# Kernel optimization log

Hardware: AMD Instinct MI355X
Metric: run time of the kernel (lower is better)

## Reference

```python
import jax, jax.numpy as jnp
import numpy as np

EMBED = 192
D_INNER = 2 * EMBED          # expand=2
D_STATE = 4                  # low_rank
D_CONV = 4
DT_RANK = (EMBED + 15) // 16 # ceil(192/16) = 12
N_MIX = 2
RANK = 4                     # LowRankProjection rank
B_, H_, W_ = 8, 64, 64


def setup_inputs() -> dict:
    key = jax.random.key(0)
    ks = jax.random.split(key, 16)
    s = lambda *sh: 1.0 / np.sqrt(sh[-1])
    inp = {
        "x": jax.random.normal(ks[0], (B_, EMBED, H_, W_), jnp.float32),
        # stacked per-mixer Mamba params (leading dim N_MIX)
        "in_proj_w": jax.random.normal(ks[1], (N_MIX, 2 * D_INNER, EMBED), jnp.float32) * s(EMBED),
        "conv_w": jax.random.normal(ks[2], (N_MIX, D_INNER, D_CONV), jnp.float32) * s(D_CONV),
        "conv_b": jnp.zeros((N_MIX, D_INNER), jnp.float32),
        "x_proj_w": jax.random.normal(ks[3], (N_MIX, DT_RANK + 2 * D_STATE, D_INNER), jnp.float32) * s(D_INNER),
        "dt_proj_w": jax.random.normal(ks[4], (N_MIX, D_INNER, DT_RANK), jnp.float32) * s(DT_RANK),
        "dt_proj_b": jax.random.uniform(ks[5], (N_MIX, D_INNER), jnp.float32, -4.0, -2.0),
        "A_log": jnp.tile(jnp.log(jnp.arange(1, D_STATE + 1, dtype=jnp.float32))[None, None, :], (N_MIX, D_INNER, 1)),
        "D": jnp.ones((N_MIX, D_INNER), jnp.float32),
        "out_proj_w": jax.random.normal(ks[6], (N_MIX, EMBED, D_INNER), jnp.float32) * s(D_INNER),
        # LowRankProjection
        "U_w": jax.random.normal(ks[7], (RANK, EMBED), jnp.float32) * s(EMBED),
        "V_w": jax.random.normal(ks[8], (EMBED, RANK), jnp.float32) * s(RANK),
        # LayerNorm
        "ln_g": jnp.ones((EMBED,), jnp.float32),
        "ln_b": jnp.zeros((EMBED,), jnp.float32),
    }
    return inp


def _silu(x):
    return x * jax.nn.sigmoid(x)


def _mamba(x, in_proj_w, conv_w, conv_b, x_proj_w, dt_proj_w, dt_proj_b, A_log, D, out_proj_w):
    # x: (B, L, d_model)
    B, L, _ = x.shape
    xz = jnp.einsum("bld,ed->ble", x, in_proj_w)          # (B, L, 2*d_inner)
    xin, z = jnp.split(xz, 2, axis=-1)
    # causal depthwise conv over L
    xt = jnp.transpose(xin, (0, 2, 1))                      # (B, d_inner, L)
    xc = jax.lax.conv_general_dilated(
        xt, conv_w[:, None, :], window_strides=(1,), padding=[(D_CONV - 1, 0)],
        feature_group_count=D_INNER, dimension_numbers=("NCH", "OIH", "NCH"))
    xa = _silu(jnp.transpose(xc + conv_b[None, :, None], (0, 2, 1)))  # (B, L, d_inner)
    x_dbl = jnp.einsum("bld,ed->ble", xa, x_proj_w)         # (B, L, dt_rank+2*d_state)
    dt_lr = x_dbl[..., :DT_RANK]
    Bm = x_dbl[..., DT_RANK:DT_RANK + D_STATE]              # (B, L, d_state)
    Cm = x_dbl[..., DT_RANK + D_STATE:]                     # (B, L, d_state)
    dt = jax.nn.softplus(jnp.einsum("blr,dr->bld", dt_lr, dt_proj_w) + dt_proj_b)  # (B, L, d_inner)
    A = -jnp.exp(A_log)                                     # (d_inner, d_state)
    dA = jnp.exp(dt[..., None] * A)                         # (B, L, d_inner, d_state)
    dBu = dt[..., None] * Bm[:, :, None, :] * xa[..., None]  # (B, L, d_inner, d_state)

    def step(h, inputs):
        dA_i, dBu_i, C_i = inputs                           # (B,d_inner,d_state),(B,d_inner,d_state),(B,d_state)
        h = dA_i * h + dBu_i
        y = jnp.einsum("bds,bs->bd", h, C_i)
        return h, y

    h0 = jnp.zeros((B, D_INNER, D_STATE), x.dtype)
    _, ys = jax.lax.scan(step, h0, (jnp.moveaxis(dA, 1, 0), jnp.moveaxis(dBu, 1, 0), jnp.moveaxis(Cm, 1, 0)))
    y = jnp.moveaxis(ys, 0, 1) + xa * D                     # (B, L, d_inner)
    y = y * _silu(z)
    return jnp.einsum("ble,de->bld", y, out_proj_w)         # (B, L, d_model)


def reference(x, in_proj_w, conv_w, conv_b, x_proj_w, dt_proj_w, dt_proj_b,
              A_log, D, out_proj_w, U_w, V_w, ln_g, ln_b):
    residual = x
    B, C, H, W = x.shape
    h = jnp.transpose(x, (0, 2, 3, 1)).reshape(B, H * W, C)
    for i in range(N_MIX):
        h = _mamba(h, in_proj_w[i], conv_w[i], conv_b[i], x_proj_w[i], dt_proj_w[i],
                   dt_proj_b[i], A_log[i], D[i], out_proj_w[i])
    # low-rank projection
    h = jnp.einsum("blr,dr->bld", jnp.einsum("blc,rc->blr", h, U_w), V_w)
    h = jnp.transpose(h.reshape(B, H, W, C), (0, 3, 1, 2)) + residual
    # LayerNorm over channels
    hc = jnp.transpose(h, (0, 2, 3, 1))
    mu = hc.mean(-1, keepdims=True)
    var = ((hc - mu) ** 2).mean(-1, keepdims=True)
    hc = (hc - mu) * jax.lax.rsqrt(var + 1e-5) * ln_g + ln_b
    return jnp.transpose(hc, (0, 3, 1, 2))
```

## Files before the change

### kernel.cpp

```cpp
#include <hip/hip_runtime.h>
#include <hip/hip_bf16.h>
#include <cstdint>

#define EMBED   192
#define DINNER  384
#define DSTATE  4
#define DCONV   4
#define DTRANK  12
#define NMIX    2
#define RANK    4
#define BB      8
#define LL      4096
#define NBL     (BB*LL)
#define NCHUNK  128
#define CLEN    32

typedef __attribute__((ext_vector_type(8))) short short8;
typedef __attribute__((ext_vector_type(4))) float float4v;

static __device__ __forceinline__ ushort f2b(float f) {
    __hip_bfloat16 h = __float2bfloat16(f);
    return *(ushort*)&h;
}
static __device__ __forceinline__ float b2f(ushort u) {
    __hip_bfloat16 h;
    *(ushort*)&h = u;
    return __bfloat162float(h);
}
static __device__ __forceinline__ float bs2f(short s) {
    ushort u = (ushort)s;
    return b2f(u);
}

__global__ __launch_bounds__(256) void k_cast(const float* __restrict__ src,
                                              ushort* __restrict__ dst, int n) {
    int i = blockIdx.x * 256 + threadIdx.x;
    if (i < n) dst[i] = f2b(src[i]);
}

__global__ __launch_bounds__(256) void k_pad_xpw(const float* __restrict__ src,
                                                 ushort* __restrict__ dst) {
    int i = blockIdx.x * 256 + threadIdx.x;
    if (i >= NMIX * 32 * 384) return;
    int mix = i / (32 * 384);
    int rem = i % (32 * 384);
    int e = rem / 384, k = rem % 384;
    dst[i] = (e < 20) ? f2b(src[(size_t)mix * 20 * 384 + e * 384 + k]) : (ushort)0;
}

__global__ __launch_bounds__(256) void k_pad_dtw(const float* __restrict__ src,
                                                 ushort* __restrict__ dst) {
    int i = blockIdx.x * 256 + threadIdx.x;
    if (i >= NMIX * 384 * 32) return;
    int mix = i / (384 * 32);
    int rem = i % (384 * 32);
    int n = rem / 32, r = rem % 32;
    dst[i] = (r < DTRANK) ? f2b(src[(size_t)mix * 384 * DTRANK + n * DTRANK + r]) : (ushort)0;
}

__global__ __launch_bounds__(256) void k_prep_cwt(const float* __restrict__ src,
                                                  float* __restrict__ dst) {
    int i = blockIdx.x * 256 + threadIdx.x;
    if (i >= NMIX * DCONV * DINNER) return;
    int mix = i / (DCONV * DINNER);
    int rem = i % (DCONV * DINNER);
    int k = rem / DINNER, d = rem % DINNER;
    dst[i] = src[(size_t)mix * DINNER * DCONV + d * DCONV + k];
}

__global__ __launch_bounds__(256) void k_transpose(const float* __restrict__ x,
                                                   ushort* __restrict__ h0b) {
    __shared__ float tile[32][33];
    int b  = blockIdx.z;
    int c0 = blockIdx.y * 32;
    int l0 = blockIdx.x * 32;
    int tx = threadIdx.x;
    int ty = threadIdx.y;
    #pragma unroll
    for (int i = 0; i < 4; i++) {
        int c = c0 + ty + i * 8;
        tile[ty + i * 8][tx] = x[((size_t)b * EMBED + c) * LL + l0 + tx];
    }
    __syncthreads();
    #pragma unroll
    for (int i = 0; i < 4; i++) {
        int l = l0 + ty + i * 8;
        h0b[((size_t)b * LL + l) * EMBED + c0 + tx] = f2b(tile[tx][ty + i * 8]);
    }
}

template<int TN, int WRN>
__global__ __launch_bounds__(256) void k_gemm_bf16(const ushort* __restrict__ A, int lda,
                                                   const ushort* __restrict__ Bw, int ldb,
                                                   float* __restrict__ C, int ldc,
                                                   ushort* __restrict__ Cb, int ldcb,
                                                   int K) {
    constexpr int WRM = 4 / WRN;
    constexpr int WM  = 128 / WRM;
    constexpr int MT  = WM / 16;
    __shared__ ushort As[128][40];
    __shared__ ushort Bs[TN][40];
    int tid  = threadIdx.x;
    int lane = tid & 63;
    int wave = tid >> 6;
    int wmo = (wave / WRN) * WM;
    int wno = (wave % WRN) * 64;
    int m0 = blockIdx.y * 128;
    int n0 = blockIdx.x * TN;

    float4v acc[MT][4];
    #pragma unroll
    for (int i = 0; i < MT; i++)
        #pragma unroll
        for (int j = 0; j < 4; j++)
            acc[i][j] = (float4v){0.f, 0.f, 0.f, 0.f};

    for (int k0 = 0; k0 < K; k0 += 32) {
        #pragma unroll
        for (int i = 0; i < 2; i++) {
            int idx = tid + i * 256;
            int r = idx >> 2, sg = idx & 3;
            *(short8*)&As[r][sg * 8] =
                *(const short8*)(A + (size_t)(m0 + r) * lda + k0 + sg * 8);
        }
        #pragma unroll
        for (int i = 0; i < TN / 64; i++) {
            int idx = tid + i * 256;
            int r = idx >> 2, sg = idx & 3;
            *(short8*)&Bs[r][sg * 8] =
                *(const short8*)(Bw + (size_t)(n0 + r) * ldb + k0 + sg * 8);
        }
        __syncthreads();
        short8 av[MT], bv[4];
        #pragma unroll
        for (int i = 0; i < MT; i++)
            av[i] = *(const short8*)&As[wmo + i * 16 + (lane & 15)][(lane >> 4) * 8];
        #pragma unroll
        for (int j = 0; j < 4; j++)
            bv[j] = *(const short8*)&Bs[wno + j * 16 + (lane & 15)][(lane >> 4) * 8];
        #pragma unroll
        for (int i = 0; i < MT; i++)
            #pragma unroll
            for (int j = 0; j < 4; j++)
                acc[i][j] = __builtin_amdgcn_mfma_f32_16x16x32_bf16(
                    av[i], bv[j], acc[i][j], 0, 0, 0);
        __syncthreads();
    }

    #pragma unroll
    for (int i = 0; i < MT; i++) {
        int rbase = m0 + wmo + i * 16 + (lane >> 4) * 4;
        #pragma unroll
        for (int j = 0; j < 4; j++) {
            int col = n0 + wno + j * 16 + (lane & 15);
            #pragma unroll
            for (int r = 0; r < 4; r++) {
                float v = acc[i][j][r];
                if (C)  C[(size_t)(rbase + r) * ldc + col] = v;
                if (Cb) Cb[(size_t)(rbase + r) * ldcb + col] = f2b(v);
            }
        }
    }
}

__global__ __launch_bounds__(256) void k_conv_silu(const ushort* __restrict__ xz,
                                                   const float* __restrict__ cwt,
                                                   const float* __restrict__ cb,
                                                   ushort* __restrict__ xa) {
    int t   = blockIdx.x * 256 + threadIdx.x;
    int g   = t % 48;
    int blc = t / 48;
    int d0  = g * 8;
    int lc  = blc % (LL / 8);
    int b   = blc / (LL / 8);
    int l0  = lc * 8;

    float wk[4][8], bias[8];
    #pragma unroll
    for (int k = 0; k < 4; k++) {
        float4v wa = *(const float4v*)(cwt + k * DINNER + d0);
        float4v wb = *(const float4v*)(cwt + k * DINNER + d0 + 4);
        #pragma unroll
        for (int j = 0; j < 4; j++) { wk[k][j] = wa[j]; wk[k][j + 4] = wb[j]; }
    }
    {
        float4v ba = *(const float4v*)(cb + d0);
        float4v bb = *(const float4v*)(cb + d0 + 4);
        #pragma unroll
        for (int j = 0; j < 4; j++) { bias[j] = ba[j]; bias[j + 4] = bb[j]; }
    }

    float r0[8] = {}, r1[8] = {}, r2[8] = {};
    const ushort* px = xz + ((size_t)(b * LL + l0)) * 768 + d0;
    if (l0 > 0) {
        short8 v;
        v = *(const short8*)(px - 3 * 768);
        #pragma unroll
        for (int j = 0; j < 8; j++) r0[j] = bs2f(v[j]);
        v = *(const short8*)(px - 2 * 768);
        #pragma unroll
        for (int j = 0; j < 8; j++) r1[j] = bs2f(v[j]);
        v = *(const short8*)(px - 1 * 768);
        #pragma unroll
        for (int j = 0; j < 8; j++) r2[j] = bs2f(v[j]);
    }
    ushort* po = xa + ((size_t)(b * LL + l0)) * DINNER + d0;
    #pragma unroll
    for (int i = 0; i < 8; i++) {
        short8 v = *(const short8*)(px + (size_t)i * 768);
        float cur[8];
        #pragma unroll
        for (int j = 0; j < 8; j++) cur[j] = bs2f(v[j]);
        short8 ov;
        #pragma unroll
        for (int j = 0; j < 8; j++) {
            float a = bias[j] + wk[0][j] * r0[j] + wk[1][j] * r1[j]
                    + wk[2][j] * r2[j] + wk[3][j] * cur[j];
            float sv = a / (1.f + __expf(-a));
            ov[j] = (short)f2b(sv);
        }
        *(short8*)(po + (size_t)i * DINNER) = ov;
        #pragma unroll
        for (int j = 0; j < 8; j++) { r0[j] = r1[j]; r1[j] = r2[j]; r2[j] = cur[j]; }
    }
}

__global__ __launch_bounds__(256) void k_xproj_mfma(const ushort* __restrict__ xa,
                                                    const ushort* __restrict__ xpwb,
                                                    float* __restrict__ xdb32,
                                                    ushort* __restrict__ xdb16) {
    __shared__ ushort As[128][40];
    __shared__ ushort Bs[32][40];
    int tid  = threadIdx.x;
    int lane = tid & 63;
    int wave = tid >> 6;
    int m0 = blockIdx.x * 128;
    float4v acc[2][2];
    #pragma unroll
    for (int i = 0; i < 2; i++)
        #pragma unroll
        for (int j = 0; j < 2; j++)
            acc[i][j] = (float4v){0.f, 0.f, 0.f, 0.f};
    for (int k0 = 0; k0 < 384; k0 += 32) {
        #pragma unroll
        for (int i = 0; i < 2; i++) {
            int idx = tid + i * 256;
            int r = idx >> 2, sg = idx & 3;
            *(short8*)&As[r][sg * 8] =
                *(const short8*)(xa + (size_t)(m0 + r) * 384 + k0 + sg * 8);
        }
        if (tid < 128) {
            int r = tid >> 2, sg = tid & 3;
            *(short8*)&Bs[r][sg * 8] =
                *(const short8*)(xpwb + (size_t)r * 384 + k0 + sg * 8);
        }
        __syncthreads();
        short8 av[2], bv[2];
        #pragma unroll
        for (int i = 0; i < 2; i++)
            av[i] = *(const short8*)&As[wave * 32 + i * 16 + (lane & 15)][(lane >> 4) * 8];
        #pragma unroll
        for (int j = 0; j < 2; j++)
            bv[j] = *(const short8*)&Bs[j * 16 + (lane & 15)][(lane >> 4) * 8];
        #pragma unroll
        for (int i = 0; i < 2; i++)
            #pragma unroll
            for (int j = 0; j < 2; j++)
                acc[i][j] = __builtin_amdgcn_mfma_f32_16x16x32_bf16(
                    av[i], bv[j], acc[i][j], 0, 0, 0);
        __syncthreads();
    }
    #pragma unroll
    for (int i = 0; i < 2; i++) {
        int rbase = m0 + wave * 32 + i * 16 + (lane >> 4) * 4;
        #pragma unroll
        for (int j = 0; j < 2; j++) {
            int col = j * 16 + (lane & 15);
            #pragma unroll
            for (int r = 0; r < 4; r++) {
                float v = acc[i][j][r];
                xdb32[(size_t)(rbase + r) * 32 + col] = v;
                xdb16[(size_t)(rbase + r) * 32 + col] = f2b(v);
            }
        }
    }
}

__global__ __launch_bounds__(256) void k_dtgemm(const ushort* __restrict__ xdb16,
                                                const ushort* __restrict__ dtwpad,
                                                const float* __restrict__ dtb,
                                                ushort* __restrict__ dtv) {
    int lane = threadIdx.x & 63;
    int wave = threadIdx.x >> 6;
    int m0 = blockIdx.x * 64 + wave * 16;
    int ak = (lane >> 4) * 8;
    short8 av = *(const short8*)(xdb16 + (size_t)(m0 + (lane & 15)) * 32 + ak);
    int rbase = m0 + (lane >> 4) * 4;
    #pragma unroll
    for (int j = 0; j < 24; j++) {
        int col = j * 16 + (lane & 15);
        short8 bv = *(const short8*)(dtwpad + (size_t)col * 32 + ak);
        float4v acc = (float4v){0.f, 0.f, 0.f, 0.f};
        acc = __builtin_amdgcn_mfma_f32_16x16x32_bf16(av, bv, acc, 0, 0, 0);
        float bias = dtb[col];
        #pragma unroll
        for (int r = 0; r < 4; r++) {
            float s = acc[r] + bias;
            float sp = fmaxf(s, 0.f) + __logf(1.f + __expf(-fabsf(s)));
            dtv[(size_t)(rbase + r) * DINNER + col] = f2b(sp);
        }
    }
}

__global__ __launch_bounds__(384) void k_scan_local(const ushort* __restrict__ xa,
                                                    const float* __restrict__ xdb32,
                                                    const ushort* __restrict__ dtvb,
                                                    const float* __restrict__ A_log,
                                                    float* __restrict__ carryT,
                                                    float* __restrict__ carryH) {
    int d     = threadIdx.x;
    int chunk = blockIdx.x;
    int b     = blockIdx.y;
    __shared__ float rows[CLEN * 32];
    size_t rbase = ((size_t)b * LL + (size_t)chunk * CLEN) * 32;
    for (int i = d; i < CLEN * 32; i += 384) rows[i] = xdb32[rbase + i];
    float As[DSTATE];
    #pragma unroll
    for (int s = 0; s < DSTATE; s++) As[s] = -__expf(A_log[d * DSTATE + s]);
    __syncthreads();
    float h[DSTATE] = {0.f, 0.f, 0.f, 0.f};
    float T = 0.f;
    size_t mbase = (size_t)b * LL + (size_t)chunk * CLEN;
    for (int l = 0; l < CLEN; l++) {
        size_t m = mbase + l;
        float dtvv = b2f(dtvb[m * DINNER + d]);
        float xav  = b2f(xa[m * DINNER + d]);
        float du   = dtvv * xav;
        T += dtvv;
        const float* row = &rows[l * 32];
        #pragma unroll
        for (int s = 0; s < DSTATE; s++) {
            float da = __expf(dtvv * As[s]);
            h[s] = da * h[s] + du * row[DTRANK + s];
        }
    }
    size_t cb = ((size_t)chunk * BB + b);
    carryT[cb * 384 + d] = T;
    float4v hv = {h[0], h[1], h[2], h[3]};
    *(float4v*)(carryH + cb * 1536 + d * 4) = hv;
}

__global__ __launch_bounds__(256) void k_scan_combine(const float* __restrict__ carryT,
                                                      const float* __restrict__ carryH,
                                                      const float* __restrict__ A_log,
                                                      float* __restrict__ carryI) {
    int c   = blockIdx.x * 256 + threadIdx.x;
    int b   = c / 1536;
    int rem = c - b * 1536;
    int d   = rem >> 2;
    float As = -__expf(A_log[rem]);
    float hrun = 0.f;
    for (int k = 0; k < NCHUNK; k++) {
        size_t o = (size_t)k * BB + b;
        float T  = carryT[o * 384 + d];
        float Hk = carryH[o * 1536 + rem];
        carryI[o * 1536 + rem] = hrun;
        hrun = __expf(As * T) * hrun + Hk;
    }
}

__global__ __launch_bounds__(384) void k_scan_final(const ushort* __restrict__ xa,
                                                    const ushort* __restrict__ xz,
                                                    const float* __restrict__ xdb32,
                                                    const ushort* __restrict__ dtvb,
                                                    const float* __restrict__ A_log,
                                                    const float* __restrict__ Dp,
                                                    const float* __restrict__ carryI,
                                                    ushort* __restrict__ y) {
    int d     = threadIdx.x;
    int chunk = blockIdx.x;
    int b     = blockIdx.y;
    __shared__ float rows[CLEN * 32];
    size_t rbase = ((size_t)b * LL + (size_t)chunk * CLEN) * 32;
    for (int i = d; i < CLEN * 32; i += 384) rows[i] = xdb32[rbase + i];
    float As[DSTATE];
    #pragma unroll
    for (int s = 0; s < DSTATE; s++) As[s] = -__expf(A_log[d * DSTATE + s]);
    float Dd = Dp[d];
    float4v hv = *(const float4v*)(carryI + ((size_t)chunk * BB + b) * 1536 + d * 4);
    float h[DSTATE];
    #pragma unroll
    for (int s = 0; s < DSTATE; s++) h[s] = hv[s];
    __syncthreads();
    size_t mbase = (size_t)b * LL + (size_t)chunk * CLEN;
    for (int l = 0; l < CLEN; l++) {
        size_t m = mbase + l;
        float dtvv = b2f(dtvb[m * DINNER + d]);
        float xav  = b2f(xa[m * DINNER + d]);
        float du   = dtvv * xav;
        const float* row = &rows[l * 32];
        float yv = 0.f;
        #pragma unroll
        for (int s = 0; s < DSTATE; s++) {
            float da = __expf(dtvv * As[s]);
            h[s] = da * h[s] + du * row[DTRANK + s];
            yv  += h[s] * row[DTRANK + DSTATE + s];
        }
        yv += xav * Dd;
        float zv = b2f(xz[m * 768 + DINNER + d]);
        yv *= zv / (1.f + __expf(-zv));
        y[m * DINNER + d] = f2b(yv);
    }
}

__global__ __launch_bounds__(256) void k_tail(const ushort* __restrict__ h1b,
                                              const float* __restrict__ x,
                                              const float* __restrict__ U,
                                              const float* __restrict__ V,
                                              const float* __restrict__ g,
                                              const float* __restrict__ be,
                                              float* __restrict__ out) {
    __shared__ float tile[EMBED * 65];
    int tid  = threadIdx.x;
    int lane = tid & 63;
    int wave = tid >> 6;
    int b  = blockIdx.y;
    int l0 = blockIdx.x * 64;
    for (int i = tid; i < EMBED * 64; i += 256) {
        int c = i >> 6, l = i & 63;
        tile[c * 65 + l] = x[((size_t)(b * EMBED + c)) * LL + l0 + l];
    }
    __syncthreads();
    for (int t = 0; t < 16; t++) {
        int lloc = wave * 16 + t;
        size_t m = (size_t)b * LL + l0 + lloc;
        float hv[3];
        #pragma unroll
        for (int i = 0; i < 3; i++) hv[i] = b2f(h1b[m * EMBED + lane + 64 * i]);
        float r[RANK];
        #pragma unroll
        for (int j = 0; j < RANK; j++) {
            float p = 0.f;
            #pragma unroll
            for (int i = 0; i < 3; i++) p += hv[i] * U[j * EMBED + lane + 64 * i];
            #pragma unroll
            for (int off = 1; off < 64; off <<= 1) p += __shfl_xor(p, off);
            r[j] = p;
        }
        float u[3], s1 = 0.f, s2 = 0.f;
        #pragma unroll
        for (int i = 0; i < 3; i++) {
            int c = lane + 64 * i;
            float v = r[0] * V[c * 4 + 0] + r[1] * V[c * 4 + 1]
                    + r[2] * V[c * 4 + 2] + r[3] * V[c * 4 + 3];
            u[i] = v + tile[c * 65 + lloc];
            s1 += u[i];
            s2 += u[i] * u[i];
        }
        #pragma unroll
        for (int off = 1; off < 64; off <<= 1) {
            s1 += __shfl_xor(s1, off);
            s2 += __shfl_xor(s2, off);
        }
        float mean = s1 * (1.f / EMBED);
        float var  = s2 * (1.f / EMBED) - mean * mean;
        float inv  = rsqrtf(var + 1e-5f);
        #pragma unroll
        for (int i = 0; i < 3; i++) {
            int c = lane + 64 * i;
            tile[c * 65 + lloc] = (u[i] - mean) * inv * g[c] + be[c];
        }
    }
    __syncthreads();
    for (int i = tid; i < EMBED * 64; i += 256) {
        int c = i >> 6, l = i & 63;
        out[((size_t)(b * EMBED + c)) * LL + l0 + l] = tile[c * 65 + l];
    }
}

extern "C" void kernel_launch(void* const* d_in, const int* in_sizes, int n_in,
                              void* d_out, int out_size, void* d_ws, size_t ws_size,
                              hipStream_t stream) {
    const float* x          = (const float*)d_in[0];
    const float* in_proj_w  = (const float*)d_in[1];
    const float* conv_w     = (const float*)d_in[2];
    const float* conv_b     = (const float*)d_in[3];
    const float* x_proj_w   = (const float*)d_in[4];
    const float* dt_proj_w  = (const float*)d_in[5];
    const float* dt_proj_b  = (const float*)d_in[6];
    const float* A_log      = (const float*)d_in[7];
    const float* Dp         = (const float*)d_in[8];
    const float* out_proj_w = (const float*)d_in[9];
    const float* U_w        = (const float*)d_in[10];
    const float* V_w        = (const float*)d_in[11];
    const float* ln_g       = (const float*)d_in[12];
    const float* ln_b       = (const float*)d_in[13];
    float* out = (float*)d_out;

    float* ws    = (float*)d_ws;
    float* xdb32 = ws;
    float* carryT = xdb32 + (size_t)NBL * 32;
    float* carryH = carryT + (size_t)NCHUNK * BB * DINNER;
    float* carryI = carryH + (size_t)NCHUNK * BB * DINNER * DSTATE;
    ushort* dtv    = (ushort*)(carryI + (size_t)NCHUNK * BB * DINNER * DSTATE);
    ushort* xz16   = dtv    + (size_t)NBL * DINNER;
    ushort* xa16   = xz16   + (size_t)NBL * 768;
    ushort* yb     = xa16   + (size_t)NBL * DINNER;
    ushort* h0b    = yb     + (size_t)NBL * DINNER;
    ushort* h1b    = h0b    + (size_t)NBL * EMBED;
    ushort* wi     = h1b    + (size_t)NBL * EMBED;
    ushort* wo     = wi     + (size_t)NMIX * 768 * EMBED;
    ushort* xpwb   = wo     + (size_t)NMIX * EMBED * DINNER;
    ushort* dtwpad = xpwb   + (size_t)NMIX * 32 * 384;
    float*  cwt    = (float*)(dtwpad + (size_t)NMIX * 384 * 32);

    const int n_wi = NMIX * 768 * EMBED;
    const int n_wo = NMIX * EMBED * DINNER;
    k_cast<<<(n_wi + 255) / 256, 256, 0, stream>>>(in_proj_w, wi, n_wi);
    k_cast<<<(n_wo + 255) / 256, 256, 0, stream>>>(out_proj_w, wo, n_wo);
    k_pad_xpw<<<(NMIX * 32 * 384 + 255) / 256, 256, 0, stream>>>(x_proj_w, xpwb);
    k_pad_dtw<<<(NMIX * 384 * 32 + 255) / 256, 256, 0, stream>>>(dt_proj_w, dtwpad);
    k_prep_cwt<<<(NMIX * DCONV * DINNER + 255) / 256, 256, 0, stream>>>(conv_w, cwt);

    k_transpose<<<dim3(LL / 32, EMBED / 32, BB), dim3(32, 8), 0, stream>>>(x, h0b);

    const ushort* hinb = h0b;
    for (int mix = 0; mix < NMIX; mix++) {
        const float* Alg = A_log + (size_t)mix * DINNER * DSTATE;

        k_gemm_bf16<128, 2><<<dim3(768 / 128, NBL / 128), 256, 0, stream>>>(
            hinb, EMBED, wi + (size_t)mix * 768 * EMBED, EMBED,
            (float*)nullptr, 0, xz16, 768, EMBED);
        k_conv_silu<<<(NBL / 8 * 48) / 256, 256, 0, stream>>>(
            xz16, cwt + (size_t)mix * DCONV * DINNER, conv_b + mix * DINNER, xa16);
        ushort* xdb16 = yb;
        k_xproj_mfma<<<NBL / 128, 256, 0, stream>>>(
            xa16, xpwb + (size_t)mix * 32 * 384, xdb32, xdb16);
        k_dtgemm<<<NBL / 64, 256, 0, stream>>>(
            xdb16, dtwpad + (size_t)mix * 384 * 32, dt_proj_b + mix * DINNER, dtv);
        k_scan_local<<<dim3(NCHUNK, BB), 384, 0, stream>>>(
            xa16, xdb32, dtv, Alg, carryT, carryH);
        k_scan_combine<<<(BB * DINNER * DSTATE) / 256, 256, 0, stream>>>(
            carryT, carryH, Alg, carryI);
        k_scan_final<<<dim3(NCHUNK, BB), 384, 0, stream>>>(
            xa16, xz16, xdb32, dtv, Alg, Dp + mix * DINNER, carryI, yb);
        k_gemm_bf16<64, 1><<<dim3(EMBED / 64, NBL / 128), 256, 0, stream>>>(
            yb, DINNER, wo + (size_t)mix * EMBED * DINNER, DINNER,
            (float*)nullptr, 0, h1b, EMBED, DINNER);
        hinb = h1b;
    }

    k_tail<<<dim3(LL / 64, BB), 256, 0, stream>>>(h1b, x, U_w, V_w, ln_g, ln_b, out);
}
```

Baseline: 428.7 us.

## Fuse weight prep kernels, fuse x_proj with dt_proj, read residual from bf16 copy

Merges the five weight cast and pad kernels into one launch. Fuses the x_proj GEMM with the dt_proj GEMM and softplus by staging the bf16 x_proj output in shared memory, so the intermediate no longer goes through global memory and one launch per mixer is removed. The tail kernel now reads the residual from the already-transposed bf16 copy h0b instead of re-transposing the fp32 input through shared memory. The residual therefore carries bf16 rounding, which lowers output accuracy.

```diff
diff --git a/kernel.cpp b/kernel.cpp
--- a/kernel.cpp
+++ b/kernel.cpp
@@ -32,40 +32,55 @@
     return b2f(u);
 }
 
-__global__ __launch_bounds__(256) void k_cast(const float* __restrict__ src,
-                                              ushort* __restrict__ dst, int n) {
+#define PREP_N0 294912
+#define PREP_N1 147456
+#define PREP_N2 24576
+#define PREP_N3 24576
+#define PREP_N4 3072
+__global__ __launch_bounds__(256) void k_prep(const float* __restrict__ in_proj_w,
+                                              const float* __restrict__ out_proj_w,
+                                              const float* __restrict__ x_proj_w,
+                                              const float* __restrict__ dt_proj_w,
+                                              const float* __restrict__ conv_w,
+                                              ushort* __restrict__ wi,
+                                              ushort* __restrict__ wo,
+                                              ushort* __restrict__ xpwb,
+                                              ushort* __restrict__ dtwpad,
+                                              float* __restrict__ cwt) {
     int i = blockIdx.x * 256 + threadIdx.x;
-    if (i < n) dst[i] = f2b(src[i]);
-}
-
-__global__ __launch_bounds__(256) void k_pad_xpw(const float* __restrict__ src,
-                                                 ushort* __restrict__ dst) {
-    int i = blockIdx.x * 256 + threadIdx.x;
-    if (i >= NMIX * 32 * 384) return;
-    int mix = i / (32 * 384);
-    int rem = i % (32 * 384);
-    int e = rem / 384, k = rem % 384;
-    dst[i] = (e < 20) ? f2b(src[(size_t)mix * 20 * 384 + e * 384 + k]) : (ushort)0;
-}
-
-__global__ __launch_bounds__(256) void k_pad_dtw(const float* __restrict__ src,
-                                                 ushort* __restrict__ dst) {
-    int i = blockIdx.x * 256 + threadIdx.x;
-    if (i >= NMIX * 384 * 32) return;
-    int mix = i / (384 * 32);
-    int rem = i % (384 * 32);
-    int n = rem / 32, r = rem % 32;
-    dst[i] = (r < DTRANK) ? f2b(src[(size_t)mix * 384 * DTRANK + n * DTRANK + r]) : (ushort)0;
-}
-
-__global__ __launch_bounds__(256) void k_prep_cwt(const float* __restrict__ src,
-                                                  float* __restrict__ dst) {
-    int i = blockIdx.x * 256 + threadIdx.x;
-    if (i >= NMIX * DCONV * DINNER) return;
-    int mix = i / (DCONV * DINNER);
-    int rem = i % (DCONV * DINNER);
-    int k = rem / DINNER, d = rem % DINNER;
-    dst[i] = src[(size_t)mix * DINNER * DCONV + d * DCONV + k];
+    if (i < PREP_N0) {
+        wi[i] = f2b(in_proj_w[i]);
+        return;
+    }
+    i -= PREP_N0;
+    if (i < PREP_N1) {
+        wo[i] = f2b(out_proj_w[i]);
+        return;
+    }
+    i -= PREP_N1;
+    if (i < PREP_N2) {
+        int mix = i / (32 * 384);
+        int rem = i % (32 * 384);
+        int e = rem / 384, k = rem % 384;
+        xpwb[i] = (e < 20) ? f2b(x_proj_w[(size_t)mix * 20 * 384 + e * 384 + k]) : (ushort)0;
+        return;
+    }
+    i -= PREP_N2;
+    if (i < PREP_N3) {
+        int mix = i / (384 * 32);
+        int rem = i % (384 * 32);
+        int n = rem / 32, r = rem % 32;
+        dtwpad[i] = (r < DTRANK) ? f2b(dt_proj_w[(size_t)mix * 384 * DTRANK + n * DTRANK + r])
+                                 : (ushort)0;
+        return;
+    }
+    i -= PREP_N3;
+    if (i < PREP_N4) {
+        int mix = i / (DCONV * DINNER);
+        int rem = i % (DCONV * DINNER);
+        int k = rem / DINNER, d = rem % DINNER;
+        cwt[i] = conv_w[(size_t)mix * DINNER * DCONV + d * DCONV + k];
+    }
 }
 
 __global__ __launch_bounds__(256) void k_transpose(const float* __restrict__ x,
@@ -225,12 +240,15 @@
     }
 }
 
-__global__ __launch_bounds__(256) void k_xproj_mfma(const ushort* __restrict__ xa,
-                                                    const ushort* __restrict__ xpwb,
-                                                    float* __restrict__ xdb32,
-                                                    ushort* __restrict__ xdb16) {
+__global__ __launch_bounds__(256) void k_xproj_dt(const ushort* __restrict__ xa,
+                                                  const ushort* __restrict__ xpwb,
+                                                  const ushort* __restrict__ dtwpad,
+                                                  const float* __restrict__ dtb,
+                                                  float* __restrict__ xdb32,
+                                                  ushort* __restrict__ dtv) {
     __shared__ ushort As[128][40];
     __shared__ ushort Bs[32][40];
+    __shared__ ushort Xs[128][40];
     int tid  = threadIdx.x;
     int lane = tid & 63;
     int wave = tid >> 6;
@@ -272,42 +290,38 @@
     }
     #pragma unroll
     for (int i = 0; i < 2; i++) {
-        int rbase = m0 + wave * 32 + i * 16 + (lane >> 4) * 4;
+        int rloc = wave * 32 + i * 16 + (lane >> 4) * 4;
         #pragma unroll
         for (int j = 0; j < 2; j++) {
             int col = j * 16 + (lane & 15);
             #pragma unroll
             for (int r = 0; r < 4; r++) {
                 float v = acc[i][j][r];
-                xdb32[(size_t)(rbase + r) * 32 + col] = v;
-                xdb16[(size_t)(rbase + r) * 32 + col] = f2b(v);
+                xdb32[(size_t)(m0 + rloc + r) * 32 + col] = v;
+                Xs[rloc + r][col] = f2b(v);
             }
         }
     }
-}
-
-__global__ __launch_bounds__(256) void k_dtgemm(const ushort* __restrict__ xdb16,
-                                                const ushort* __restrict__ dtwpad,
-                                                const float* __restrict__ dtb,
-                                                ushort* __restrict__ dtv) {
-    int lane = threadIdx.x & 63;
-    int wave = threadIdx.x >> 6;
-    int m0 = blockIdx.x * 64 + wave * 16;
+    __syncthreads();
     int ak = (lane >> 4) * 8;
-    short8 av = *(const short8*)(xdb16 + (size_t)(m0 + (lane & 15)) * 32 + ak);
-    int rbase = m0 + (lane >> 4) * 4;
-    #pragma unroll
-    for (int j = 0; j < 24; j++) {
-        int col = j * 16 + (lane & 15);
-        short8 bv = *(const short8*)(dtwpad + (size_t)col * 32 + ak);
-        float4v acc = (float4v){0.f, 0.f, 0.f, 0.f};
-        acc = __builtin_amdgcn_mfma_f32_16x16x32_bf16(av, bv, acc, 0, 0, 0);
-        float bias = dtb[col];
-        #pragma unroll
-        for (int r = 0; r < 4; r++) {
-            float s = acc[r] + bias;
-            float sp = fmaxf(s, 0.f) + __logf(1.f + __expf(-fabsf(s)));
-            dtv[(size_t)(rbase + r) * DINNER + col] = f2b(sp);
+    #pragma unroll
+    for (int rt = 0; rt < 2; rt++) {
+        int rowb = wave * 32 + rt * 16;
+        short8 av = *(const short8*)&Xs[rowb + (lane & 15)][ak];
+        int rbase = m0 + rowb + (lane >> 4) * 4;
+        #pragma unroll
+        for (int j = 0; j < 24; j++) {
+            int col = j * 16 + (lane & 15);
+            short8 bv = *(const short8*)(dtwpad + (size_t)col * 32 + ak);
+            float4v dacc = (float4v){0.f, 0.f, 0.f, 0.f};
+            dacc = __builtin_amdgcn_mfma_f32_16x16x32_bf16(av, bv, dacc, 0, 0, 0);
+            float bias = dtb[col];
+            #pragma unroll
+            for (int r = 0; r < 4; r++) {
+                float s = dacc[r] + bias;
+                float sp = fmaxf(s, 0.f) + __logf(1.f + __expf(-fabsf(s)));
+                dtv[(size_t)(rbase + r) * DINNER + col] = f2b(sp);
+            }
         }
     }
 }
@@ -414,7 +428,7 @@
 }
 
 __global__ __launch_bounds__(256) void k_tail(const ushort* __restrict__ h1b,
-                                              const float* __restrict__ x,
+                                              const ushort* __restrict__ h0b,
                                               const float* __restrict__ U,
                                               const float* __restrict__ V,
                                               const float* __restrict__ g,
@@ -426,11 +440,6 @@
     int wave = tid >> 6;
     int b  = blockIdx.y;
     int l0 = blockIdx.x * 64;
-    for (int i = tid; i < EMBED * 64; i += 256) {
-        int c = i >> 6, l = i & 63;
-        tile[c * 65 + l] = x[((size_t)(b * EMBED + c)) * LL + l0 + l];
-    }
-    __syncthreads();
     for (int t = 0; t < 16; t++) {
         int lloc = wave * 16 + t;
         size_t m = (size_t)b * LL + l0 + lloc;
@@ -453,7 +462,7 @@
             int c = lane + 64 * i;
             float v = r[0] * V[c * 4 + 0] + r[1] * V[c * 4 + 1]
                     + r[2] * V[c * 4 + 2] + r[3] * V[c * 4 + 3];
-            u[i] = v + tile[c * 65 + lloc];
+            u[i] = v + b2f(h0b[m * EMBED + c]);
             s1 += u[i];
             s2 += u[i] * u[i];
         }
@@ -514,13 +523,8 @@
     ushort* dtwpad = xpwb   + (size_t)NMIX * 32 * 384;
     float*  cwt    = (float*)(dtwpad + (size_t)NMIX * 384 * 32);
 
-    const int n_wi = NMIX * 768 * EMBED;
-    const int n_wo = NMIX * EMBED * DINNER;
-    k_cast<<<(n_wi + 255) / 256, 256, 0, stream>>>(in_proj_w, wi, n_wi);
-    k_cast<<<(n_wo + 255) / 256, 256, 0, stream>>>(out_proj_w, wo, n_wo);
-    k_pad_xpw<<<(NMIX * 32 * 384 + 255) / 256, 256, 0, stream>>>(x_proj_w, xpwb);
-    k_pad_dtw<<<(NMIX * 384 * 32 + 255) / 256, 256, 0, stream>>>(dt_proj_w, dtwpad);
-    k_prep_cwt<<<(NMIX * DCONV * DINNER + 255) / 256, 256, 0, stream>>>(conv_w, cwt);
+    k_prep<<<(PREP_N0 + PREP_N1 + PREP_N2 + PREP_N3 + PREP_N4) / 256, 256, 0, stream>>>(
+        in_proj_w, out_proj_w, x_proj_w, dt_proj_w, conv_w, wi, wo, xpwb, dtwpad, cwt);
 
     k_transpose<<<dim3(LL / 32, EMBED / 32, BB), dim3(32, 8), 0, stream>>>(x, h0b);
 
@@ -533,11 +537,9 @@
             (float*)nullptr, 0, xz16, 768, EMBED);
         k_conv_silu<<<(NBL / 8 * 48) / 256, 256, 0, stream>>>(
             xz16, cwt + (size_t)mix * DCONV * DINNER, conv_b + mix * DINNER, xa16);
-        ushort* xdb16 = yb;
-        k_xproj_mfma<<<NBL / 128, 256, 0, stream>>>(
-            xa16, xpwb + (size_t)mix * 32 * 384, xdb32, xdb16);
-        k_dtgemm<<<NBL / 64, 256, 0, stream>>>(
-            xdb16, dtwpad + (size_t)mix * 384 * 32, dt_proj_b + mix * DINNER, dtv);
+        k_xproj_dt<<<NBL / 128, 256, 0, stream>>>(
+            xa16, xpwb + (size_t)mix * 32 * 384, dtwpad + (size_t)mix * 384 * 32,
+            dt_proj_b + mix * DINNER, xdb32, dtv);
         k_scan_local<<<dim3(NCHUNK, BB), 384, 0, stream>>>(
             xa16, xdb32, dtv, Alg, carryT, carryH);
         k_scan_combine<<<(BB * DINNER * DSTATE) / 256, 256, 0, stream>>>(
@@ -550,5 +552,5 @@
         hinb = h1b;
     }
 
-    k_tail<<<dim3(LL / 64, BB), 256, 0, stream>>>(h1b, x, U_w, V_w, ln_g, ln_b, out);
-}
+    k_tail<<<dim3(LL / 64, BB), 256, 0, stream>>>(h1b, h0b, U_w, V_w, ln_g, ln_b, out);
+}
```

Measured after the change: 437.4 us. +2.0%, slower.
